# Performance work log

Hardware: AMD Instinct MI355X
Metric: run time of the kernel (lower is better)

Reference implementation:

```python
import jax, jax.numpy as jnp
import numpy as np

INDEX_SHIFT = jnp.array([[0, 0], [-1, 0], [1, 0], [0, 1], [-1, 1], [1, 1], [0, -1], [-1, -1], [1, -1]], dtype=jnp.int32)
H, W = 320, 320
C = 32          # embed_dim / feat_channels (hard-coded 32 in module)
NH = 2          # head_num
HD = C // NH    # per-head dim
B, N = 4, 20000


def setup_inputs() -> dict:
    key = jax.random.key(0)
    ks = jax.random.split(key, 8)

    def coords(k):
        # unique (y, x) coords per sample so the coord->index lookup is well defined
        perm = jax.random.permutation(k, H * W)[:N]
        return jnp.stack([perm // W, perm % W], axis=-1).astype(jnp.int32)

    li_coors = jax.vmap(coords)(jax.random.split(ks[0], B))
    ra_coors = jax.vmap(coords)(jax.random.split(ks[1], B))
    li_feats = jax.random.normal(ks[2], (B, N, C), jnp.float32)
    ra_feats = jax.random.normal(ks[3], (B, N, C), jnp.float32)
    pos = jax.random.normal(ks[4], (9, C), jnp.float32) * 0.02

    s = 1.0 / np.sqrt(C)
    out = {"li_bev_feats": li_feats, "li_bev_coors": li_coors,
           "ra_bev_feats": ra_feats, "ra_bev_coors": ra_coors,
           "pos_embedding": pos}
    for i, kk in [(1, ks[5]), (2, ks[6])]:
        k0, k1 = jax.random.split(kk)
        out[f"in_w{i}"] = jax.random.uniform(k0, (3 * C, C), jnp.float32, -s, s)
        out[f"in_b{i}"] = jnp.zeros((3 * C,), jnp.float32)
        out[f"out_w{i}"] = jax.random.uniform(k1, (C, C), jnp.float32, -s, s)
        out[f"out_b{i}"] = jnp.zeros((C,), jnp.float32)
    return out


def _build_kv(q_coors, kv_coors, kv_feats, pos):
    # q_coors, kv_coors: (N,2) int; kv_feats: (N,C)
    n = q_coors.shape[0]
    grid = jnp.full((H * W,), -1, jnp.int32)
    grid = grid.at[kv_coors[:, 0] * W + kv_coors[:, 1]].set(jnp.arange(n, dtype=jnp.int32))
    sc = q_coors[None, :, :] + INDEX_SHIFT[:, None, :]            # (9,N,2)
    valid = (sc[..., 0] >= 0) & (sc[..., 0] < H) & (sc[..., 1] >= 0) & (sc[..., 1] < W)
    flat = jnp.clip(sc[..., 0], 0, H - 1) * W + jnp.clip(sc[..., 1], 0, W - 1)
    sel = jnp.where(valid, grid[flat], -1)                        # (9,N)
    mask = (sel >= 0)[..., None]                                  # (9,N,1)
    g = kv_feats[jnp.maximum(sel, 0)]                             # (9,N,C)
    k = jnp.where(mask, g, 0.0)
    v = jnp.where(mask, g + pos[:, None, :], 0.0)
    return k.transpose(1, 0, 2), v.transpose(1, 0, 2)             # (N,9,C)


def _mha(q, k, v, in_w, in_b, out_w, out_b):
    # q: (N,C); k,v: (N,L,C). torch MultiheadAttention (eval mode, dropout off).
    n, L = k.shape[0], k.shape[1]
    wq, wk, wv = in_w[:C], in_w[C:2 * C], in_w[2 * C:]
    bq, bk, bv = in_b[:C], in_b[C:2 * C], in_b[2 * C:]
    qh = (q @ wq.T + bq).reshape(n, NH, HD)
    kh = (k @ wk.T + bk).reshape(n, L, NH, HD)
    vh = (v @ wv.T + bv).reshape(n, L, NH, HD)
    scores = jnp.einsum('nhd,nlhd->nhl', qh, kh) / np.sqrt(HD)
    attn = jax.nn.softmax(scores, axis=-1)
    o = jnp.einsum('nhl,nlhd->nhd', attn, vh).reshape(n, C)
    return o @ out_w.T + out_b


def _scatter(feats, coors):
    # PointPillarsScatter: place (N,C) feats at (y,x) into a (C,H,W) canvas
    idx = coors[:, 0] * W + coors[:, 1]
    canvas = jnp.zeros((C, H * W), feats.dtype)
    return canvas.at[:, idx].set(feats.T).reshape(C, H, W)


def reference(li_bev_feats, li_bev_coors, ra_bev_feats, ra_bev_coors, pos_embedding,
              in_w1, in_b1, out_w1, out_b1, in_w2, in_b2, out_w2, out_b2):
    def one(li_f, li_c, ra_f, ra_c):
        k, v = _build_kv(li_c, ra_c, ra_f, pos_embedding)
        li_img = _scatter(_mha(li_f, k, v, in_w1, in_b1, out_w1, out_b1), li_c)
        k, v = _build_kv(ra_c, li_c, li_f, pos_embedding)
        ra_img = _scatter(_mha(ra_f, k, v, in_w2, in_b2, out_w2, out_b2), ra_c)
        return li_img, ra_img
    li_imgs, ra_imgs = jax.vmap(one)(li_bev_feats, li_bev_coors, ra_bev_feats, ra_bev_coors)
    return li_imgs, ra_imgs  # each (B, C, H, W)
```

## Files before the change

kernel.cpp:

```cpp
#include <hip/hip_runtime.h>
#include <hip/hip_fp16.h>

constexpr int Hh = 320, Ww = 320, Cc = 32, Bb = 4, Nn = 20000;
constexpr int HWp = Hh * Ww;

__device__ __forceinline__ float4 shfl_xor4(float4 v, int m) {
  return make_float4(__shfl_xor(v.x, m), __shfl_xor(v.y, m),
                     __shfl_xor(v.z, m), __shfl_xor(v.w, m));
}

template <int CTRL>
__device__ __forceinline__ float dpp_mov(float x) {
  return __int_as_float(
      __builtin_amdgcn_update_dpp(0, __float_as_int(x), CTRL, 0xF, 0xF, true));
}
template <int CTRL>
__device__ __forceinline__ float4 dpp_mov4(float4 v) {
  return make_float4(dpp_mov<CTRL>(v.x), dpp_mov<CTRL>(v.y),
                     dpp_mov<CTRL>(v.z), dpp_mov<CTRL>(v.w));
}
__device__ __forceinline__ float quad_add_xor1(float x) {
  return x + dpp_mov<0xB1>(x);
}
__device__ __forceinline__ float quad_add_xor2(float x) {
  return x + dpp_mov<0x4E>(x);
}

union H4 { __half2 h2[2]; float2 f2; };
union H8 { __half2 h2[4]; float4 f4; };

__device__ __forceinline__ void store_h4(__half* p, float4 v) {
  H4 u;
  u.h2[0] = __floats2half2_rn(v.x, v.y);
  u.h2[1] = __floats2half2_rn(v.z, v.w);
  *(float2*)p = u.f2;
}
__device__ __forceinline__ float4 cvt_h4(float2 raw) {
  H4 u;
  u.f2 = raw;
  float2 lo = __half22float2(u.h2[0]), hi = __half22float2(u.h2[1]);
  return make_float4(lo.x, lo.y, hi.x, hi.y);
}

__global__ __launch_bounds__(256) void prep_k(
    int* __restrict__ grids, const float* __restrict__ pos,
    const float* __restrict__ in_w1, const float* __restrict__ in_w2,
    float* __restrict__ posv) {
  int bx = blockIdx.x;
  if (bx < 800) {
    int i = bx * 256 + threadIdx.x;
    ((int4*)grids)[i] = make_int4(-1, -1, -1, -1);
    return;
  }
  int t = (bx - 800) * 256 + threadIdx.x;
  if (t >= 2 * 9 * Cc) return;
  int dir = t / (9 * Cc);
  int rem = t - dir * 9 * Cc;
  int l = rem / Cc, ch = rem - l * Cc;
  const float* w = (dir == 0 ? in_w1 : in_w2) + (2 * Cc + ch) * Cc;
  const float* pl = pos + l * Cc;
  float acc = 0.f;
  for (int j = 0; j < Cc; j++) acc += pl[j] * w[j];
  posv[t] = acc;
}

constexpr int PROJ_BLOCKS_PER_SB = 157;
constexpr int PROJ_TOTAL = PROJ_BLOCKS_PER_SB * 8;
constexpr int BUILD_BLOCKS = 625;

__global__ __launch_bounds__(256) void project_build_k(
    const float* __restrict__ li_feats, const float* __restrict__ ra_feats,
    const int* __restrict__ li_coors, const int* __restrict__ ra_coors,
    const float* __restrict__ in_w1, const float* __restrict__ in_b1,
    const float* __restrict__ in_w2, const float* __restrict__ in_b2,
    __half* __restrict__ Qh, __half* __restrict__ Kp, __half* __restrict__ Vp,
    int* __restrict__ grids) {
  int bx = blockIdx.x;
  if (bx >= PROJ_TOTAL) {
    int idx = (bx - PROJ_TOTAL) * 256 + threadIdx.x;
    int src = idx / (Bb * Nn);
    int r = idx - src * (Bb * Nn);
    int b = r / Nn, n = r - b * Nn;
    const int* c = (src == 0 ? li_coors : ra_coors) + ((size_t)b * Nn + n) * 2;
    grids[((size_t)src * Bb + b) * HWp + c[0] * Ww + c[1]] = n;
    return;
  }
  int sb = bx / PROJ_BLOCKS_PER_SB;
  int blk = bx - sb * PROJ_BLOCKS_PER_SB;
  int src = sb >> 2, b = sb & 3;
  __shared__ __align__(16) float wqT[32 * 36];
  __shared__ __align__(16) float wkT[32 * 36];
  __shared__ __align__(16) float wvT[32 * 36];
  __shared__ float bq[Cc];
  const float* wA = src == 0 ? in_w1 : in_w2;
  const float* bA = src == 0 ? in_b1 : in_b2;
  const float* wB = src == 0 ? in_w2 : in_w1;
  int t = threadIdx.x;
  for (int i = t; i < Cc * Cc; i += 256) {
    int c = i >> 5, j = i & 31;
    wqT[j * 36 + c] = wA[i];
    wkT[j * 36 + c] = wB[Cc * Cc + i];
    wvT[j * 36 + c] = wB[2 * Cc * Cc + i];
  }
  if (t < Cc) bq[t] = bA[t];
  __syncthreads();
  int quad = t >> 3, c4 = t & 7;
  int n0 = blk * 128 + quad * 4;
  if (n0 + 4 > Nn) n0 = Nn - 4;
  const float* f = (src == 0 ? li_feats : ra_feats) + ((size_t)b * Nn + n0) * Cc;
  const float4* wq4 = (const float4*)wqT;
  const float4* wk4 = (const float4*)wkT;
  const float4* wv4 = (const float4*)wvT;
  float4 bq4 = *(const float4*)(bq + c4 * 4);
  float4 aq[4], ak[4], av[4];
#pragma unroll
  for (int i = 0; i < 4; i++) {
    aq[i] = bq4;
    ak[i] = make_float4(0.f, 0.f, 0.f, 0.f);
    av[i] = make_float4(0.f, 0.f, 0.f, 0.f);
  }
#pragma unroll
  for (int j4 = 0; j4 < 8; j4++) {
    float fjs[4][4];
#pragma unroll
    for (int i = 0; i < 4; i++) {
      float4 v = ((const float4*)(f + i * Cc))[j4];
      fjs[i][0] = v.x; fjs[i][1] = v.y; fjs[i][2] = v.z; fjs[i][3] = v.w;
    }
#pragma unroll
    for (int u = 0; u < 4; u++) {
      int j = j4 * 4 + u;
      float4 q4 = wq4[j * 9 + c4];
      float4 k4 = wk4[j * 9 + c4];
      float4 v4 = wv4[j * 9 + c4];
#pragma unroll
      for (int i = 0; i < 4; i++) {
        float fj = fjs[i][u];
        aq[i].x += fj * q4.x; aq[i].y += fj * q4.y;
        aq[i].z += fj * q4.z; aq[i].w += fj * q4.w;
        ak[i].x += fj * k4.x; ak[i].y += fj * k4.y;
        ak[i].z += fj * k4.z; ak[i].w += fj * k4.w;
        av[i].x += fj * v4.x; av[i].y += fj * v4.y;
        av[i].z += fj * v4.z; av[i].w += fj * v4.w;
      }
    }
  }
  int dirkv = 1 - src;
  size_t qbase = (((size_t)src * Bb + b) * Nn + n0) * Cc + c4 * 4;
  size_t kvbase = (((size_t)dirkv * Bb + b) * Nn + n0) * Cc + c4 * 4;
#pragma unroll
  for (int i = 0; i < 4; i++) {
    store_h4(Qh + qbase + i * Cc, aq[i]);
    store_h4(Kp + kvbase + i * Cc, ak[i]);
    store_h4(Vp + kvbase + i * Cc, av[i]);
  }
}

__global__ __launch_bounds__(256) void attn8_k(
    const int* __restrict__ li_coors, const int* __restrict__ ra_coors,
    const int* __restrict__ grids, const __half* __restrict__ Qh,
    const __half* __restrict__ Kp, const __half* __restrict__ Vp,
    const float* __restrict__ posv, const float* __restrict__ in_b1,
    const float* __restrict__ in_b2, const float* __restrict__ out_w1,
    const float* __restrict__ out_b1, const float* __restrict__ out_w2,
    const float* __restrict__ out_b2, __half* __restrict__ out_pts) {
  int db = blockIdx.y;
  int dir = db >> 2, b = db & 3;
  __shared__ __align__(16) float ow[Cc * Cc];
  __shared__ __align__(16) float pv[9 * Cc];
  __shared__ float sbk[Cc], sbv[Cc], sob[Cc];
  const float* owp = dir == 0 ? out_w1 : out_w2;
  const float* obp = dir == 0 ? out_b1 : out_b2;
  const float* ibp = dir == 0 ? in_b1 : in_b2;
  int t = threadIdx.x;
  for (int i = t; i < Cc * Cc; i += 256) ow[i] = owp[i];
  for (int i = t; i < 9 * Cc; i += 256) pv[i] = posv[dir * 9 * Cc + i];
  if (t < Cc) {
    sbk[t] = ibp[Cc + t];
    sbv[t] = ibp[2 * Cc + t];
    sob[t] = obp[t];
  }
  __syncthreads();
  int pt = t >> 3, c4 = t & 7;
  int n = blockIdx.x * 32 + pt;
  const int2* qcp =
      (const int2*)((dir == 0 ? li_coors : ra_coors) + (size_t)b * Nn * 2);
  int2 yx = qcp[n];
  int y = yx.x, x = yx.y;
  const int* g = grids + ((size_t)(1 - dir) * Bb + b) * HWp;
  const int DY[9] = {0, -1, 1, 0, -1, 1, 0, -1, 1};
  const int DX[9] = {0, 0, 0, 1, 1, 1, -1, -1, -1};
  int sel[9];
#pragma unroll
  for (int l = 0; l < 9; l++) {
    int cy = y + DY[l], cx = x + DX[l];
    sel[l] = ((unsigned)cy < (unsigned)Hh && (unsigned)cx < (unsigned)Ww)
                 ? g[cy * Ww + cx]
                 : -1;
  }
  const __half* Kpb = Kp + ((size_t)dir * Bb + b) * Nn * Cc;
  const __half* Vpb = Vp + ((size_t)dir * Bb + b) * Nn * Cc;
  float2 kr[9], vr[9];
#pragma unroll
  for (int l = 0; l < 9; l++) {
    float2 kk = make_float2(0.f, 0.f);
    float2 vv = make_float2(0.f, 0.f);
    int se = sel[l];
    if (se >= 0) {
      kk = *(const float2*)(Kpb + (size_t)se * Cc + c4 * 4);
      vv = *(const float2*)(Vpb + (size_t)se * Cc + c4 * 4);
    }
    kr[l] = kk;
    vr[l] = vv;
  }
  float4 qh4 = cvt_h4(
      *(const float2*)(Qh + (((size_t)dir * Bb + b) * Nn + n) * Cc + c4 * 4));
  float4 bk4 = *(const float4*)(sbk + c4 * 4);
  float pb = qh4.x * bk4.x + qh4.y * bk4.y + qh4.z * bk4.z + qh4.w * bk4.w;
  pb = quad_add_xor1(pb);
  pb = quad_add_xor2(pb);
  float s[9];
#pragma unroll
  for (int l = 0; l < 9; l++) {
    float4 k4 = cvt_h4(kr[l]);
    float d = qh4.x * k4.x + qh4.y * k4.y + qh4.z * k4.z + qh4.w * k4.w;
    d = quad_add_xor1(d);
    d = quad_add_xor2(d);
    s[l] = 0.25f * (pb + d);
  }
  float m = s[0];
#pragma unroll
  for (int l = 1; l < 9; l++) m = fmaxf(m, s[l]);
  float sum = 0.f;
#pragma unroll
  for (int l = 0; l < 9; l++) {
    s[l] = __expf(s[l] - m);
    sum += s[l];
  }
  float4 o4 = make_float4(0.f, 0.f, 0.f, 0.f);
#pragma unroll
  for (int l = 0; l < 9; l++) {
    float wp = (sel[l] >= 0) ? s[l] : 0.f;
    float4 v4 = cvt_h4(vr[l]);
    float4 p4 = *(const float4*)(pv + l * Cc + c4 * 4);
    o4.x += wp * (v4.x + p4.x);
    o4.y += wp * (v4.y + p4.y);
    o4.z += wp * (v4.z + p4.z);
    o4.w += wp * (v4.w + p4.w);
  }
  float r = 1.f / sum;
  float4 bv4 = *(const float4*)(sbv + c4 * 4);
  o4 = make_float4(o4.x * r + bv4.x, o4.y * r + bv4.y, o4.z * r + bv4.z,
                   o4.w * r + bv4.w);
  const float4* ow4 = (const float4*)ow;
  float4 sob4 = *(const float4*)(sob + c4 * 4);
  float acc0 = sob4.x, acc1 = sob4.y, acc2 = sob4.z, acc3 = sob4.w;
#define OUTPROJ_ACC(OJ, JB)                                            \
  {                                                                    \
    float4 oj = (OJ);                                                  \
    int jb = (JB);                                                     \
    float4 w0 = ow4[(c4 * 4 + 0) * 8 + jb];                            \
    float4 w1 = ow4[(c4 * 4 + 1) * 8 + jb];                            \
    float4 w2 = ow4[(c4 * 4 + 2) * 8 + jb];                            \
    float4 w3 = ow4[(c4 * 4 + 3) * 8 + jb];                            \
    acc0 += oj.x * w0.x + oj.y * w0.y + oj.z * w0.z + oj.w * w0.w;     \
    acc1 += oj.x * w1.x + oj.y * w1.y + oj.z * w1.z + oj.w * w1.w;     \
    acc2 += oj.x * w2.x + oj.y * w2.y + oj.z * w2.z + oj.w * w2.w;     \
    acc3 += oj.x * w3.x + oj.y * w3.y + oj.z * w3.z + oj.w * w3.w;     \
  }
  OUTPROJ_ACC(o4, c4);
  OUTPROJ_ACC(dpp_mov4<0xB1>(o4), c4 ^ 1);
  OUTPROJ_ACC(dpp_mov4<0x4E>(o4), c4 ^ 2);
  OUTPROJ_ACC(dpp_mov4<0x1B>(o4), c4 ^ 3);
  float4 o4s = shfl_xor4(o4, 4);
  OUTPROJ_ACC(o4s, c4 ^ 4);
  OUTPROJ_ACC(dpp_mov4<0xB1>(o4s), c4 ^ 5);
  OUTPROJ_ACC(dpp_mov4<0x4E>(o4s), c4 ^ 6);
  OUTPROJ_ACC(dpp_mov4<0x1B>(o4s), c4 ^ 7);
#undef OUTPROJ_ACC
  store_h4(out_pts + (((size_t)dir * Bb + b) * Nn + n) * Cc + c4 * 4,
           make_float4(acc0, acc1, acc2, acc3));
}

__global__ __launch_bounds__(256) void scatter_k(
    const int* __restrict__ grids, const __half* __restrict__ out_pts,
    float* __restrict__ out) {
  int db = blockIdx.y;
  int dir = db >> 2, b = db & 3;
  int p = blockIdx.x * 256 + threadIdx.x;
  const int* gq = grids + ((size_t)dir * Bb + b) * HWp;
  int se = gq[p];
  float* ob = out + (((size_t)dir * Bb + b) * Cc) * HWp + p;
  if (se < 0) {
#pragma unroll
    for (int c = 0; c < Cc; c++) ob[(size_t)c * HWp] = 0.f;
  } else {
    const float4* sp =
        (const float4*)(out_pts + (((size_t)dir * Bb + b) * Nn + se) * Cc);
#pragma unroll
    for (int c8 = 0; c8 < 4; c8++) {
      H8 u;
      u.f4 = sp[c8];
#pragma unroll
      for (int k = 0; k < 4; k++) {
        float2 pr = __half22float2(u.h2[k]);
        ob[(size_t)(c8 * 8 + k * 2 + 0) * HWp] = pr.x;
        ob[(size_t)(c8 * 8 + k * 2 + 1) * HWp] = pr.y;
      }
    }
  }
}

extern "C" void kernel_launch(void* const* d_in, const int* in_sizes, int n_in,
                              void* d_out, int out_size, void* d_ws, size_t ws_size,
                              hipStream_t stream) {
  const float* li_feats = (const float*)d_in[0];
  const int* li_coors = (const int*)d_in[1];
  const float* ra_feats = (const float*)d_in[2];
  const int* ra_coors = (const int*)d_in[3];
  const float* pos = (const float*)d_in[4];
  const float* in_w1 = (const float*)d_in[5];
  const float* in_b1 = (const float*)d_in[6];
  const float* out_w1 = (const float*)d_in[7];
  const float* out_b1 = (const float*)d_in[8];
  const float* in_w2 = (const float*)d_in[9];
  const float* in_b2 = (const float*)d_in[10];
  const float* out_w2 = (const float*)d_in[11];
  const float* out_b2 = (const float*)d_in[12];

  char* ws = (char*)d_ws;
  size_t off = 0;
  int* grids = (int*)(ws + off);
  off += (size_t)2 * Bb * HWp * 4;
  __half* Qh = (__half*)(ws + off);
  off += (size_t)2 * Bb * Nn * Cc * 2;
  __half* Kp = (__half*)(ws + off);
  off += (size_t)2 * Bb * Nn * Cc * 2;
  __half* Vp = (__half*)(ws + off);
  off += (size_t)2 * Bb * Nn * Cc * 2;
  __half* out_pts = (__half*)(ws + off);
  off += (size_t)2 * Bb * Nn * Cc * 2;
  float* posv = (float*)(ws + off);
  off += 2 * 9 * Cc * 4;

  prep_k<<<803, 256, 0, stream>>>(grids, pos, in_w1, in_w2, posv);
  project_build_k<<<PROJ_TOTAL + BUILD_BLOCKS, 256, 0, stream>>>(
      li_feats, ra_feats, li_coors, ra_coors, in_w1, in_b1, in_w2, in_b2, Qh, Kp,
      Vp, grids);
  dim3 ga(Nn / 32, 2 * Bb);
  attn8_k<<<ga, 256, 0, stream>>>(li_coors, ra_coors, grids, Qh, Kp, Vp, posv,
                                  in_b1, in_b2, out_w1, out_b1, out_w2, out_b2,
                                  out_pts);
  dim3 gs(HWp / 256, 2 * Bb);
  scatter_k<<<gs, 256, 0, stream>>>(grids, out_pts, (float*)d_out);
}
```

Before: 89.02 us.

## Fold output projection into per-head value projection weights

Precomputes per-head products of the output projection and value projection (plus the projected positional embedding and the combined bias) in the prep kernel. The projection kernel then emits two per-head pre-projected value tensors, so the attention kernel drops its out-projection matmul and cross-lane shuffles and simply mixes the two head-specific value vectors with the softmax weights. The trade is one extra fp16 value tensor to write and gather per neighbour, which means more memory traffic in the gather-bound attention kernel. Rounding also changes because the folded products are stored in fp16.

```diff
diff --git a/kernel.cpp b/kernel.cpp
--- a/kernel.cpp
+++ b/kernel.cpp
@@ -3,21 +3,11 @@
 
 constexpr int Hh = 320, Ww = 320, Cc = 32, Bb = 4, Nn = 20000;
 constexpr int HWp = Hh * Ww;
-
-__device__ __forceinline__ float4 shfl_xor4(float4 v, int m) {
-  return make_float4(__shfl_xor(v.x, m), __shfl_xor(v.y, m),
-                     __shfl_xor(v.z, m), __shfl_xor(v.w, m));
-}
 
 template <int CTRL>
 __device__ __forceinline__ float dpp_mov(float x) {
   return __int_as_float(
       __builtin_amdgcn_update_dpp(0, __float_as_int(x), CTRL, 0xF, 0xF, true));
-}
-template <int CTRL>
-__device__ __forceinline__ float4 dpp_mov4(float4 v) {
-  return make_float4(dpp_mov<CTRL>(v.x), dpp_mov<CTRL>(v.y),
-                     dpp_mov<CTRL>(v.z), dpp_mov<CTRL>(v.w));
 }
 __device__ __forceinline__ float quad_add_xor1(float x) {
   return x + dpp_mov<0xB1>(x);
@@ -44,24 +34,52 @@
 
 __global__ __launch_bounds__(256) void prep_k(
     int* __restrict__ grids, const float* __restrict__ pos,
-    const float* __restrict__ in_w1, const float* __restrict__ in_w2,
-    float* __restrict__ posv) {
+    const float* __restrict__ in_w1, const float* __restrict__ in_b1,
+    const float* __restrict__ out_w1, const float* __restrict__ out_b1,
+    const float* __restrict__ in_w2, const float* __restrict__ in_b2,
+    const float* __restrict__ out_w2, const float* __restrict__ out_b2,
+    float* __restrict__ Wvo, float* __restrict__ pv2g,
+    float* __restrict__ obias2) {
   int bx = blockIdx.x;
   if (bx < 800) {
     int i = bx * 256 + threadIdx.x;
     ((int4*)grids)[i] = make_int4(-1, -1, -1, -1);
     return;
   }
-  int t = (bx - 800) * 256 + threadIdx.x;
-  if (t >= 2 * 9 * Cc) return;
-  int dir = t / (9 * Cc);
-  int rem = t - dir * 9 * Cc;
-  int l = rem / Cc, ch = rem - l * Cc;
-  const float* w = (dir == 0 ? in_w1 : in_w2) + (2 * Cc + ch) * Cc;
-  const float* pl = pos + l * Cc;
-  float acc = 0.f;
-  for (int j = 0; j < Cc; j++) acc += pl[j] * w[j];
-  posv[t] = acc;
+  int dir = bx - 800;
+  const float* iw = dir == 0 ? in_w1 : in_w2;
+  const float* ib = dir == 0 ? in_b1 : in_b2;
+  const float* owp = dir == 0 ? out_w1 : out_w2;
+  const float* obp = dir == 0 ? out_b1 : out_b2;
+  __shared__ float sow[1024], swv[1024], sW[2048];
+  int t = threadIdx.x;
+  for (int i = t; i < 1024; i += 256) {
+    sow[i] = owp[i];
+    swv[i] = iw[2 * Cc * Cc + i];
+  }
+  __syncthreads();
+  for (int e = t; e < 2048; e += 256) {
+    int h = e >> 10, idx = e & 1023;
+    int c = idx >> 5, j = idx & 31;
+    float acc = 0.f;
+    for (int jj = 0; jj < 16; jj++)
+      acc += sow[c * 32 + h * 16 + jj] * swv[(h * 16 + jj) * 32 + j];
+    sW[e] = acc;
+    Wvo[dir * 2048 + e] = acc;
+  }
+  __syncthreads();
+  for (int e = t; e < 576; e += 256) {
+    int h = e / 288, rem = e - h * 288;
+    int l = rem >> 5, c = rem & 31;
+    float acc = 0.f;
+    for (int j = 0; j < 32; j++) acc += pos[l * 32 + j] * sW[h * 1024 + c * 32 + j];
+    pv2g[dir * 576 + e] = acc;
+  }
+  if (t < Cc) {
+    float acc = obp[t];
+    for (int j = 0; j < 32; j++) acc += ib[2 * Cc + j] * sow[t * 32 + j];
+    obias2[dir * Cc + t] = acc;
+  }
 }
 
 constexpr int PROJ_BLOCKS_PER_SB = 157;
@@ -73,7 +91,9 @@
     const int* __restrict__ li_coors, const int* __restrict__ ra_coors,
     const float* __restrict__ in_w1, const float* __restrict__ in_b1,
     const float* __restrict__ in_w2, const float* __restrict__ in_b2,
-    __half* __restrict__ Qh, __half* __restrict__ Kp, __half* __restrict__ Vp,
+    const float* __restrict__ Wvo,
+    __half* __restrict__ Qh, __half* __restrict__ Kp,
+    __half* __restrict__ V0, __half* __restrict__ V1,
     int* __restrict__ grids) {
   int bx = blockIdx.x;
   if (bx >= PROJ_TOTAL) {
@@ -90,17 +110,21 @@
   int src = sb >> 2, b = sb & 3;
   __shared__ __align__(16) float wqT[32 * 36];
   __shared__ __align__(16) float wkT[32 * 36];
-  __shared__ __align__(16) float wvT[32 * 36];
+  __shared__ __align__(16) float w0T[32 * 36];
+  __shared__ __align__(16) float w1T[32 * 36];
   __shared__ float bq[Cc];
   const float* wA = src == 0 ? in_w1 : in_w2;
   const float* bA = src == 0 ? in_b1 : in_b2;
   const float* wB = src == 0 ? in_w2 : in_w1;
+  int dirkv = 1 - src;
+  const float* Wf = Wvo + (size_t)dirkv * 2048;
   int t = threadIdx.x;
   for (int i = t; i < Cc * Cc; i += 256) {
     int c = i >> 5, j = i & 31;
     wqT[j * 36 + c] = wA[i];
     wkT[j * 36 + c] = wB[Cc * Cc + i];
-    wvT[j * 36 + c] = wB[2 * Cc * Cc + i];
+    w0T[j * 36 + c] = Wf[i];
+    w1T[j * 36 + c] = Wf[1024 + i];
   }
   if (t < Cc) bq[t] = bA[t];
   __syncthreads();
@@ -110,14 +134,16 @@
   const float* f = (src == 0 ? li_feats : ra_feats) + ((size_t)b * Nn + n0) * Cc;
   const float4* wq4 = (const float4*)wqT;
   const float4* wk4 = (const float4*)wkT;
-  const float4* wv4 = (const float4*)wvT;
+  const float4* w04 = (const float4*)w0T;
+  const float4* w14 = (const float4*)w1T;
   float4 bq4 = *(const float4*)(bq + c4 * 4);
-  float4 aq[4], ak[4], av[4];
+  float4 aq[4], ak[4], a0[4], a1[4];
 #pragma unroll
   for (int i = 0; i < 4; i++) {
     aq[i] = bq4;
     ak[i] = make_float4(0.f, 0.f, 0.f, 0.f);
-    av[i] = make_float4(0.f, 0.f, 0.f, 0.f);
+    a0[i] = make_float4(0.f, 0.f, 0.f, 0.f);
+    a1[i] = make_float4(0.f, 0.f, 0.f, 0.f);
   }
 #pragma unroll
   for (int j4 = 0; j4 < 8; j4++) {
@@ -132,7 +158,8 @@
       int j = j4 * 4 + u;
       float4 q4 = wq4[j * 9 + c4];
       float4 k4 = wk4[j * 9 + c4];
-      float4 v4 = wv4[j * 9 + c4];
+      float4 v04 = w04[j * 9 + c4];
+      float4 v14 = w14[j * 9 + c4];
 #pragma unroll
       for (int i = 0; i < 4; i++) {
         float fj = fjs[i][u];
@@ -140,45 +167,41 @@
         aq[i].z += fj * q4.z; aq[i].w += fj * q4.w;
         ak[i].x += fj * k4.x; ak[i].y += fj * k4.y;
         ak[i].z += fj * k4.z; ak[i].w += fj * k4.w;
-        av[i].x += fj * v4.x; av[i].y += fj * v4.y;
-        av[i].z += fj * v4.z; av[i].w += fj * v4.w;
+        a0[i].x += fj * v04.x; a0[i].y += fj * v04.y;
+        a0[i].z += fj * v04.z; a0[i].w += fj * v04.w;
+        a1[i].x += fj * v14.x; a1[i].y += fj * v14.y;
+        a1[i].z += fj * v14.z; a1[i].w += fj * v14.w;
       }
     }
   }
-  int dirkv = 1 - src;
   size_t qbase = (((size_t)src * Bb + b) * Nn + n0) * Cc + c4 * 4;
   size_t kvbase = (((size_t)dirkv * Bb + b) * Nn + n0) * Cc + c4 * 4;
 #pragma unroll
   for (int i = 0; i < 4; i++) {
     store_h4(Qh + qbase + i * Cc, aq[i]);
     store_h4(Kp + kvbase + i * Cc, ak[i]);
-    store_h4(Vp + kvbase + i * Cc, av[i]);
+    store_h4(V0 + kvbase + i * Cc, a0[i]);
+    store_h4(V1 + kvbase + i * Cc, a1[i]);
   }
 }
 
 __global__ __launch_bounds__(256) void attn8_k(
     const int* __restrict__ li_coors, const int* __restrict__ ra_coors,
     const int* __restrict__ grids, const __half* __restrict__ Qh,
-    const __half* __restrict__ Kp, const __half* __restrict__ Vp,
-    const float* __restrict__ posv, const float* __restrict__ in_b1,
-    const float* __restrict__ in_b2, const float* __restrict__ out_w1,
-    const float* __restrict__ out_b1, const float* __restrict__ out_w2,
-    const float* __restrict__ out_b2, __half* __restrict__ out_pts) {
+    const __half* __restrict__ Kp, const __half* __restrict__ V0,
+    const __half* __restrict__ V1, const float* __restrict__ pv2g,
+    const float* __restrict__ in_b1, const float* __restrict__ in_b2,
+    const float* __restrict__ obias2, __half* __restrict__ out_pts) {
   int db = blockIdx.y;
   int dir = db >> 2, b = db & 3;
-  __shared__ __align__(16) float ow[Cc * Cc];
-  __shared__ __align__(16) float pv[9 * Cc];
-  __shared__ float sbk[Cc], sbv[Cc], sob[Cc];
-  const float* owp = dir == 0 ? out_w1 : out_w2;
-  const float* obp = dir == 0 ? out_b1 : out_b2;
+  __shared__ __align__(16) float spv[576];
+  __shared__ float sbk[Cc], sob[Cc];
   const float* ibp = dir == 0 ? in_b1 : in_b2;
   int t = threadIdx.x;
-  for (int i = t; i < Cc * Cc; i += 256) ow[i] = owp[i];
-  for (int i = t; i < 9 * Cc; i += 256) pv[i] = posv[dir * 9 * Cc + i];
+  for (int i = t; i < 576; i += 256) spv[i] = pv2g[dir * 576 + i];
   if (t < Cc) {
     sbk[t] = ibp[Cc + t];
-    sbv[t] = ibp[2 * Cc + t];
-    sob[t] = obp[t];
+    sob[t] = obias2[dir * Cc + t];
   }
   __syncthreads();
   int pt = t >> 3, c4 = t & 7;
@@ -198,20 +221,26 @@
                  ? g[cy * Ww + cx]
                  : -1;
   }
-  const __half* Kpb = Kp + ((size_t)dir * Bb + b) * Nn * Cc;
-  const __half* Vpb = Vp + ((size_t)dir * Bb + b) * Nn * Cc;
-  float2 kr[9], vr[9];
+  size_t dbb = ((size_t)dir * Bb + b) * Nn * Cc;
+  const __half* Kpb = Kp + dbb;
+  const __half* V0b = V0 + dbb;
+  const __half* V1b = V1 + dbb;
+  float2 kr[9], v0r[9], v1r[9];
 #pragma unroll
   for (int l = 0; l < 9; l++) {
     float2 kk = make_float2(0.f, 0.f);
-    float2 vv = make_float2(0.f, 0.f);
+    float2 v0v = make_float2(0.f, 0.f);
+    float2 v1v = make_float2(0.f, 0.f);
     int se = sel[l];
     if (se >= 0) {
-      kk = *(const float2*)(Kpb + (size_t)se * Cc + c4 * 4);
-      vv = *(const float2*)(Vpb + (size_t)se * Cc + c4 * 4);
+      size_t o = (size_t)se * Cc + c4 * 4;
+      kk = *(const float2*)(Kpb + o);
+      v0v = *(const float2*)(V0b + o);
+      v1v = *(const float2*)(V1b + o);
     }
     kr[l] = kk;
-    vr[l] = vv;
+    v0r[l] = v0v;
+    v1r[l] = v1v;
   }
   float4 qh4 = cvt_h4(
       *(const float2*)(Qh + (((size_t)dir * Bb + b) * Nn + n) * Cc + c4 * 4));
@@ -237,49 +266,32 @@
     s[l] = __expf(s[l] - m);
     sum += s[l];
   }
-  float4 o4 = make_float4(0.f, 0.f, 0.f, 0.f);
-#pragma unroll
-  for (int l = 0; l < 9; l++) {
-    float wp = (sel[l] >= 0) ? s[l] : 0.f;
-    float4 v4 = cvt_h4(vr[l]);
-    float4 p4 = *(const float4*)(pv + l * Cc + c4 * 4);
-    o4.x += wp * (v4.x + p4.x);
-    o4.y += wp * (v4.y + p4.y);
-    o4.z += wp * (v4.z + p4.z);
-    o4.w += wp * (v4.w + p4.w);
-  }
-  float r = 1.f / sum;
-  float4 bv4 = *(const float4*)(sbv + c4 * 4);
-  o4 = make_float4(o4.x * r + bv4.x, o4.y * r + bv4.y, o4.z * r + bv4.z,
-                   o4.w * r + bv4.w);
-  const float4* ow4 = (const float4*)ow;
-  float4 sob4 = *(const float4*)(sob + c4 * 4);
-  float acc0 = sob4.x, acc1 = sob4.y, acc2 = sob4.z, acc3 = sob4.w;
-#define OUTPROJ_ACC(OJ, JB)                                            \
-  {                                                                    \
-    float4 oj = (OJ);                                                  \
-    int jb = (JB);                                                     \
-    float4 w0 = ow4[(c4 * 4 + 0) * 8 + jb];                            \
-    float4 w1 = ow4[(c4 * 4 + 1) * 8 + jb];                            \
-    float4 w2 = ow4[(c4 * 4 + 2) * 8 + jb];                            \
-    float4 w3 = ow4[(c4 * 4 + 3) * 8 + jb];                            \
-    acc0 += oj.x * w0.x + oj.y * w0.y + oj.z * w0.z + oj.w * w0.w;     \
-    acc1 += oj.x * w1.x + oj.y * w1.y + oj.z * w1.z + oj.w * w1.w;     \
-    acc2 += oj.x * w2.x + oj.y * w2.y + oj.z * w2.z + oj.w * w2.w;     \
-    acc3 += oj.x * w3.x + oj.y * w3.y + oj.z * w3.z + oj.w * w3.w;     \
-  }
-  OUTPROJ_ACC(o4, c4);
-  OUTPROJ_ACC(dpp_mov4<0xB1>(o4), c4 ^ 1);
-  OUTPROJ_ACC(dpp_mov4<0x4E>(o4), c4 ^ 2);
-  OUTPROJ_ACC(dpp_mov4<0x1B>(o4), c4 ^ 3);
-  float4 o4s = shfl_xor4(o4, 4);
-  OUTPROJ_ACC(o4s, c4 ^ 4);
-  OUTPROJ_ACC(dpp_mov4<0xB1>(o4s), c4 ^ 5);
-  OUTPROJ_ACC(dpp_mov4<0x4E>(o4s), c4 ^ 6);
-  OUTPROJ_ACC(dpp_mov4<0x1B>(o4s), c4 ^ 7);
-#undef OUTPROJ_ACC
-  store_h4(out_pts + (((size_t)dir * Bb + b) * Nn + n) * Cc + c4 * 4,
-           make_float4(acc0, acc1, acc2, acc3));
+  float rsum = 1.f / sum;
+  float aown[9], aoth[9];
+#pragma unroll
+  for (int l = 0; l < 9; l++) aown[l] = s[l] * rsum;
+#pragma unroll
+  for (int l = 0; l < 9; l++) aoth[l] = __shfl_xor(aown[l], 4);
+  int hd = c4 >> 2;
+  float4 acc = *(const float4*)(sob + c4 * 4);
+  const float* pv0 = spv + 0 * 288 + c4 * 4;
+  const float* pv1 = spv + 1 * 288 + c4 * 4;
+#pragma unroll
+  for (int l = 0; l < 9; l++) {
+    if (sel[l] >= 0) {
+      float a0w = hd == 0 ? aown[l] : aoth[l];
+      float a1w = hd == 0 ? aoth[l] : aown[l];
+      float4 v0 = cvt_h4(v0r[l]);
+      float4 v1 = cvt_h4(v1r[l]);
+      float4 p0 = *(const float4*)(pv0 + l * 32);
+      float4 p1 = *(const float4*)(pv1 + l * 32);
+      acc.x += a0w * (v0.x + p0.x) + a1w * (v1.x + p1.x);
+      acc.y += a0w * (v0.y + p0.y) + a1w * (v1.y + p1.y);
+      acc.z += a0w * (v0.z + p0.z) + a1w * (v1.z + p1.z);
+      acc.w += a0w * (v0.w + p0.w) + a1w * (v1.w + p1.w);
+    }
+  }
+  store_h4(out_pts + (((size_t)dir * Bb + b) * Nn + n) * Cc + c4 * 4, acc);
 }
 
 __global__ __launch_bounds__(256) void scatter_k(
@@ -336,21 +348,28 @@
   off += (size_t)2 * Bb * Nn * Cc * 2;
   __half* Kp = (__half*)(ws + off);
   off += (size_t)2 * Bb * Nn * Cc * 2;
-  __half* Vp = (__half*)(ws + off);
+  __half* V0 = (__half*)(ws + off);
+  off += (size_t)2 * Bb * Nn * Cc * 2;
+  __half* V1 = (__half*)(ws + off);
   off += (size_t)2 * Bb * Nn * Cc * 2;
   __half* out_pts = (__half*)(ws + off);
   off += (size_t)2 * Bb * Nn * Cc * 2;
-  float* posv = (float*)(ws + off);
-  off += 2 * 9 * Cc * 4;
-
-  prep_k<<<803, 256, 0, stream>>>(grids, pos, in_w1, in_w2, posv);
+  float* Wvo = (float*)(ws + off);
+  off += 2 * 2048 * 4;
+  float* pv2g = (float*)(ws + off);
+  off += 2 * 576 * 4;
+  float* obias2 = (float*)(ws + off);
+  off += 2 * Cc * 4;
+
+  prep_k<<<802, 256, 0, stream>>>(grids, pos, in_w1, in_b1, out_w1, out_b1,
+                                  in_w2, in_b2, out_w2, out_b2, Wvo, pv2g,
+                                  obias2);
   project_build_k<<<PROJ_TOTAL + BUILD_BLOCKS, 256, 0, stream>>>(
-      li_feats, ra_feats, li_coors, ra_coors, in_w1, in_b1, in_w2, in_b2, Qh, Kp,
-      Vp, grids);
+      li_feats, ra_feats, li_coors, ra_coors, in_w1, in_b1, in_w2, in_b2, Wvo,
+      Qh, Kp, V0, V1, grids);
   dim3 ga(Nn / 32, 2 * Bb);
-  attn8_k<<<ga, 256, 0, stream>>>(li_coors, ra_coors, grids, Qh, Kp, Vp, posv,
-                                  in_b1, in_b2, out_w1, out_b1, out_w2, out_b2,
-                                  out_pts);
+  attn8_k<<<ga, 256, 0, stream>>>(li_coors, ra_coors, grids, Qh, Kp, V0, V1,
+                                  pv2g, in_b1, in_b2, obias2, out_pts);
   dim3 gs(HWp / 256, 2 * Bb);
   scatter_k<<<gs, 256, 0, stream>>>(grids, out_pts, (float*)d_out);
 }
```

After: 88.77 us. Within noise of the previous version (-0.3%).
